# Optimization experiments

Hardware: AMD Instinct MI355X
Metric: run time of the kernel (lower is better)

## Reference

```python
import jax, jax.numpy as jnp
import numpy as np

POOL = 7          # pool_size
RES = 42          # ROIS_resolution
CH = 2048         # backbone output channels (Xception)
GCN_DIM = 256     # gcn_outfeat_dim (== gat_outfeat_dim after head split, heads=1)
HEADS = 1
GAT_CH = 256
ALPHA = 0.1       # APPNP teleport
EPS = 1e-3        # keras BatchNormalization epsilon
CHUNKS = CH // GCN_DIM            # 8 channel chunks per ROI
CNODES = CHUNKS * POOL * POOL     # 392 intra-graph nodes


def _rois():
    # fixed ROI boxes (x, y, w, h) on the 42x42 upsampled map:
    # 3x3 grid of 14x14 cells + two horizontal halves + full image
    c = RES // 3
    r = [(x * c, y * c, c, c) for y in range(3) for x in range(3)]
    r += [(0, 0, RES, RES // 2), (0, RES // 2, RES, RES // 2), (0, 0, RES, RES)]
    return r

ROIS = _rois()
NUM_ROIS = len(ROIS)  # 12


def _gcn_adj(n):
    # spektral GCNConv.preprocess on all-ones adjacency: D^-1/2 (A + I) D^-1/2
    a = np.ones((n, n), np.float32) + np.eye(n, dtype=np.float32)
    d = a.sum(1)
    return jnp.asarray(a / np.sqrt(np.outer(d, d)))

A_INTRA = _gcn_adj(CNODES)        # (392, 392)
A_INTER = _gcn_adj(NUM_ROIS + 1)  # (13, 13)


def _appnp(x, a, w, b):
    # APPNPConv, propagations=1, sigmoid MLP: (1-a)*A@m + a*m
    m = jax.nn.sigmoid(x @ w + b)
    return (1.0 - ALPHA) * jnp.einsum('nm,...mf->...nf', a, m) + ALPHA * m


def _gat(x, a, k, a_self, a_neigh, b):
    # GATConv._call_dense (inference: dropout off); a has add_self_loops folded in
    xp = jnp.einsum('...ni,iho->...nho', x, k)          # (...,N,H,C)
    s = jnp.einsum('...nhi,iho->...nho', xp, a_self)    # (...,N,H,1)
    t = jnp.einsum('...nhi,iho->...nho', xp, a_neigh)   # (...,N,H,1)
    coef = s + jnp.swapaxes(t, -3, -1)                  # (...,N,H,N)
    coef = jax.nn.leaky_relu(coef, 0.2)
    mask = jnp.where(a == 0.0, -1e10, 0.0)              # (N,N) (all-connected here)
    coef = jax.nn.softmax(coef + mask[:, None, :], axis=-1)
    out = jnp.einsum('...nhm,...mhi->...nhi', coef, xp)
    out = out.reshape(out.shape[:-2] + (HEADS * GAT_CH,))  # concat heads
    return jax.nn.elu(out + b)


def _gnn_block(x, a, aw, ab, gk, gs, gn, gb):
    h = _appnp(x, a, aw, ab) + x
    return _gat(h, a, gk, gs, gn, gb) + h


def setup_inputs() -> dict:
    key = jax.random.key(0)
    ks = jax.random.split(key, 8)
    s = 0.05
    return {
        'base_out': jax.random.normal(ks[0], (8, POOL, POOL, CH), jnp.float32),
        'appnp_w': jax.random.normal(ks[1], (GCN_DIM, GCN_DIM), jnp.float32) * s,
        'appnp_b': jnp.zeros((GCN_DIM,), jnp.float32),
        'gat_kernel': jax.random.normal(ks[2], (GCN_DIM, HEADS, GAT_CH), jnp.float32) * s,
        'gat_attn_self': jax.random.normal(ks[3], (GAT_CH, HEADS, 1), jnp.float32) * s,
        'gat_attn_neighs': jax.random.normal(ks[4], (GAT_CH, HEADS, 1), jnp.float32) * s,
        'gat_bias': jnp.zeros((HEADS * GAT_CH,), jnp.float32),
        'pool_feat_w': jax.random.normal(ks[5], (GCN_DIM, 2 * GCN_DIM), jnp.float32) * s,
        'pool_feat_b': jnp.zeros((2 * GCN_DIM,), jnp.float32),
        'pool_attn_w': jax.random.normal(ks[6], (GCN_DIM, 2 * GCN_DIM), jnp.float32) * s,
        'pool_attn_b': jnp.zeros((2 * GCN_DIM,), jnp.float32),
        'bn_gamma': jnp.ones((2 * GCN_DIM,), jnp.float32),
        'bn_beta': jnp.zeros((2 * GCN_DIM,), jnp.float32),
        'bn_mean': jnp.zeros((2 * GCN_DIM,), jnp.float32),
        'bn_var': jnp.ones((2 * GCN_DIM,), jnp.float32),
        'dense_w': jax.random.normal(ks[7], (2 * GCN_DIM, 200), jnp.float32) * s,
        'dense_b': jnp.zeros((200,), jnp.float32),
    }


def reference(base_out, appnp_w, appnp_b, gat_kernel, gat_attn_self, gat_attn_neighs,
              gat_bias, pool_feat_w, pool_feat_b, pool_attn_w, pool_attn_b,
              bn_gamma, bn_beta, bn_mean, bn_var, dense_w, dense_b):
    B = base_out.shape[0]
    # upsample backbone features to ROI resolution
    x0 = jax.image.resize(base_out, (B, RES, RES, CH), 'bilinear')
    # RoiPoolingConv: crop each static ROI and resize to (POOL, POOL)
    pooled = [jax.image.resize(x0[:, y:y + h, x:x + w, :], (B, POOL, POOL, CH), 'bilinear')
              for (x, y, w, h) in ROIS]
    pooled.append(base_out)  # global node (pool_size == base_out spatial dim)
    rois = jnp.stack(pooled, axis=1)  # (B, R+1, 7, 7, CH)
    # _temp_nodes_transform: split channels into CHUNKS, concat along node axis
    nodes = rois.reshape(B, NUM_ROIS + 1, POOL * POOL, CHUNKS, GCN_DIM)
    nodes = nodes.transpose(0, 1, 3, 2, 4).reshape(B, NUM_ROIS + 1, CNODES, GCN_DIM)
    gnn = (appnp_w, appnp_b, gat_kernel, gat_attn_self, gat_attn_neighs, gat_bias)
    # intra-ROI graphs: 13 independent 392-node graphs (batched over (B, R+1))
    x2_intra = _gnn_block(nodes, A_INTRA, *gnn).reshape(B, (NUM_ROIS + 1) * CNODES, GCN_DIM)
    # inter-ROI graphs: 392 independent 13-node graphs
    xt = nodes.transpose(0, 2, 1, 3)  # (B, CNODES, R+1, GCN_DIM)
    x2_inter = _gnn_block(xt, A_INTER, *gnn).reshape(B, CNODES * (NUM_ROIS + 1), GCN_DIM)
    x2 = jnp.concatenate([x2_intra, x2_inter], axis=1)  # (B, 10192, 256)
    # GlobalAttentionPool(512)
    feat = x2 @ pool_feat_w + pool_feat_b
    gate = jax.nn.sigmoid(x2 @ pool_attn_w + pool_attn_b)
    xf = jnp.sum(gate * feat, axis=1)  # (B, 512)
    # BatchNorm (inference) + softmax classifier
    xn = (xf - bn_mean) / jnp.sqrt(bn_var + EPS) * bn_gamma + bn_beta
    return jax.nn.softmax(xn @ dense_w + dense_b, axis=-1)
```

## Files before the change

### kernel.cpp

```cpp
#include <hip/hip_runtime.h>
#include <math.h>


typedef __attribute__((ext_vector_type(8))) short bf16x8;
typedef __attribute__((ext_vector_type(4))) float f32x4;

#define MFMA16x32(a, b, c) __builtin_amdgcn_mfma_f32_16x16x32_bf16((a), (b), (c), 0, 0, 0)

__device__ __forceinline__ float sigmoidf_(float x) { return 1.0f / (1.0f + __expf(-x)); }
__device__ __forceinline__ float leakyf_(float x) { return x >= 0.0f ? x : 0.2f * x; }
__device__ __forceinline__ float eluf_(float x) { return x > 0.0f ? x : __expf(x) - 1.0f; }
__device__ __forceinline__ short f2bf(float f) {
  unsigned u = __builtin_bit_cast(unsigned, f);
  unsigned r = u + 0x7fffu + ((u >> 16) & 1u);
  return (short)(r >> 16);
}
__device__ __forceinline__ float bf2f(short s) {
  unsigned u = ((unsigned)(unsigned short)s) << 16;
  return __builtin_bit_cast(float, u);
}
__device__ __forceinline__ f32x4 fzero4() {
  f32x4 z;
  #pragma unroll
  for (int i = 0; i < 4; ++i) z[i] = 0.0f;
  return z;
}

#define GLDS16(g, l) __builtin_amdgcn_global_load_lds( \
    (const __attribute__((address_space(1))) void*)(g), \
    (__attribute__((address_space(3))) void*)(l), 16, 0, 0)

__global__ __launch_bounds__(256) void prep_k(
    const float* __restrict__ appnp_w, const float* __restrict__ gat_k,
    const float* __restrict__ pf_w, const float* __restrict__ pa_w,
    const float* __restrict__ gat_as, const float* __restrict__ gat_an,
    short* __restrict__ aWhi, short* __restrict__ gkhi,
    short* __restrict__ pwcomb, float* __restrict__ wtab,
    float* __restrict__ was, float* __restrict__ wan) {
  const int bx = blockIdx.x;
  const int tid = threadIdx.x;
  if (bx < 512) {
    const int idx = (bx & 255) * 256 + tid;
    const int k = idx >> 8, n = idx & 255;
    const float* src = (bx < 256) ? appnp_w : gat_k;
    short* dst = (bx < 256) ? aWhi : gkhi;
    dst[(size_t)n * 256 + k] = f2bf(src[(size_t)k * 256 + n]);
  } else if (bx < 1536) {
    const int idx = (bx - 512) * 256 + tid;
    const int n = idx >> 8, k = idx & 255;
    const int p = n >> 4, i = n & 15;
    const int sc = ((p >> 1) << 4) + i;
    const float v = (p & 1) ? pa_w[(size_t)k * 512 + sc] : pf_w[(size_t)k * 512 + sc];
    pwcomb[(size_t)n * 256 + k] = f2bf(v);
  } else if (bx == 1536) {
    const int RX[12] = {0,14,28, 0,14,28, 0,14,28, 0, 0, 0};
    const int RY[12] = {0, 0, 0,14,14,14,28,28,28, 0,21, 0};
    const int RW[12] = {14,14,14,14,14,14,14,14,14,42,42,42};
    const int RH[12] = {14,14,14,14,14,14,14,14,14,21,21,42};
    for (int e = tid; e < 13 * 2 * 49; e += 256) {
      const int roi = e / 98;
      const int rest = e % 98;
      const int axis = rest / 49;
      const int o = (rest % 49) / 7;
      const int ib = rest % 7;
      float wout;
      if (roi == 12) {
        wout = (o == ib) ? 1.0f : 0.0f;
      } else {
        const int start = axis ? RX[roi] : RY[roi];
        const int len = axis ? RW[roi] : RH[roi];
        const float s = (float)len / 7.0f;
        const float oc = (o + 0.5f) * s - 0.5f;
        float wsum = 0.0f, dot = 0.0f;
        for (int j = 0; j < len; ++j) {
          float w = 1.0f - fabsf((float)j - oc) / s;
          if (w <= 0.0f) continue;
          wsum += w;
          const float ic = ((float)(start + j) + 0.5f) / 6.0f - 0.5f;
          const float fl = floorf(ic);
          const int ia = (int)fl;
          const float fr = ic - fl;
          int c0 = ia;     if (c0 < 0) c0 = 0; if (c0 > 6) c0 = 6;
          int c1 = ia + 1; if (c1 < 0) c1 = 0; if (c1 > 6) c1 = 6;
          float u = 0.0f;
          if (c0 == ib) u += 1.0f - fr;
          if (c1 == ib) u += fr;
          dot += w * u;
        }
        wout = dot / wsum;
      }
      wtab[e] = wout;
    }
  } else {
    const int w = tid >> 6, l = tid & 63;
    const int row = (bx - 1537) * 4 + w;
    const float* p = gat_k + (size_t)row * 256;
    float s = 0.0f, t = 0.0f;
    #pragma unroll
    for (int j = 0; j < 4; ++j) {
      const int o = l + j * 64;
      const float v = p[o];
      s = fmaf(v, gat_as[o], s);
      t = fmaf(v, gat_an[o], t);
    }
    #pragma unroll
    for (int off = 32; off; off >>= 1) { s += __shfl_down(s, off); t += __shfl_down(t, off); }
    if (l == 0) { was[row] = s; wan[row] = t; }
  }
}

__global__ __launch_bounds__(256) void nodes_k(const float* __restrict__ base,
                                               const float* __restrict__ wtab,
                                               short* __restrict__ nodes) {
  const int blk = blockIdx.x;
  const int chunk = blk & 7;
  const int br = blk >> 3;
  const int r = br % 13;
  const int b = br / 13;
  const int f = threadIdx.x;
  __shared__ float W49[49][50];
  const float* wv = wtab + (r * 2 + 0) * 49;
  const float* wh = wtab + (r * 2 + 1) * 49;
  for (int e = f; e < 2401; e += 256) {
    const int o = e / 49, in = e % 49;
    W49[o][in] = wv[(o / 7) * 7 + in / 7] * wh[(o % 7) * 7 + in % 7];
  }
  __syncthreads();
  float bv[49];
  const float* bp = base + (size_t)b * 49 * 2048 + chunk * 256 + f;
  #pragma unroll
  for (int in = 0; in < 49; ++in) bv[in] = bp[(size_t)in * 2048];
  const size_t obase = ((size_t)(b * 13 + r) * 392 + chunk * 49) * 256 + f;
  for (int o = 0; o < 49; ++o) {
    float acc = 0.0f;
    #pragma unroll
    for (int in = 0; in < 49; ++in) acc = fmaf(W49[o][in], bv[in], acc);
    nodes[obase + (size_t)o * 256] = f2bf(acc);
  }
}

enum { EP_PLAIN = 0, EP_SIG = 1, EP_POOL = 3 };

template <int EPI>
__global__ __launch_bounds__(256) void gemm_t(
    const short* __restrict__ A, const short* __restrict__ BT,
    const int Kpad, const int nkt, const int Mvalid, const int segRows,
    const float* __restrict__ e0, const float* __restrict__ e1,
    short* __restrict__ Cs, float* __restrict__ xf) {
  const int tid = threadIdx.x;
  const int w = tid >> 6, l = tid & 63;
  const int lr = l & 15, kb = l >> 4;
  const int wr = w >> 1, wc = w & 1;

  int row0, col0, rbase = 0, bseg = 0;
  if constexpr (EPI == EP_POOL) {
    const int bid = blockIdx.x;
    const int eff = (bid & 7) * 640 + (bid >> 3);
    const int mt = eff >> 3, ct = eff & 7;
    row0 = mt * 128; col0 = ct * 128;
    rbase = (mt % 40) * 128;
    bseg = (mt / 40) & 7;
  } else {
    row0 = blockIdx.x * 128; col0 = blockIdx.y * 128;
  }

  __shared__ short As[128][32];
  __shared__ short Bs[128][32];

  const short* ag0 = A + (size_t)(row0 + w * 32 + (l >> 2)) * Kpad + (l & 3) * 8;
  const short* ag1 = ag0 + (size_t)16 * Kpad;
  const short* bg0 = BT + (size_t)(col0 + w * 32 + (l >> 2)) * Kpad + (l & 3) * 8;
  const short* bg1 = bg0 + (size_t)16 * Kpad;
  short* lA0 = &As[w * 32][0];
  short* lA1 = &As[w * 32 + 16][0];
  short* lB0 = &Bs[w * 32][0];
  short* lB1 = &Bs[w * 32 + 16][0];

  f32x4 acc[4][4];
  #pragma unroll
  for (int i = 0; i < 4; ++i)
    #pragma unroll
    for (int j = 0; j < 4; ++j) acc[i][j] = fzero4();

  for (int kt = 0; kt < nkt; ++kt) {
    const int ko = kt * 32;
    __syncthreads();
    GLDS16(ag0 + ko, lA0);
    GLDS16(ag1 + ko, lA1);
    GLDS16(bg0 + ko, lB0);
    GLDS16(bg1 + ko, lB1);
    __syncthreads();
    bf16x8 va[4], vb[4];
    #pragma unroll
    for (int i = 0; i < 4; ++i) va[i] = *(const bf16x8*)&As[wr * 64 + i * 16 + lr][kb * 8];
    #pragma unroll
    for (int j = 0; j < 4; ++j) vb[j] = *(const bf16x8*)&Bs[wc * 64 + j * 16 + lr][kb * 8];
    #pragma unroll
    for (int i = 0; i < 4; ++i)
      #pragma unroll
      for (int j = 0; j < 4; ++j) acc[i][j] = MFMA16x32(va[i], vb[j], acc[i][j]);
  }

  if constexpr (EPI == EP_PLAIN || EPI == EP_SIG) {
    #pragma unroll
    for (int j = 0; j < 4; ++j) {
      const int col = col0 + wc * 64 + j * 16 + lr;
      float bs = 0.0f;
      if constexpr (EPI == EP_SIG) bs = e0[col];
      #pragma unroll
      for (int i = 0; i < 4; ++i) {
        const int row = row0 + wr * 64 + i * 16 + kb * 4;
        #pragma unroll
        for (int r = 0; r < 4; ++r) {
          const int grow = row + r;
          const int lrow = (grow >= segRows) ? grow - segRows : grow;
          if (lrow < Mvalid) {
            float o = acc[i][j][r];
            if constexpr (EPI == EP_SIG) o = sigmoidf_(o + bs);
            Cs[(size_t)grow * 256 + col] = f2bf(o);
          }
        }
      }
    }
  } else {
    #pragma unroll
    for (int jp = 0; jp < 2; ++jp) {
      const int j = jp * 2;
      const int cg = col0 + wc * 64 + j * 16;
      const int realcol = ((cg >> 5) << 4) + lr;
      const float bfv = e0[realcol], bav = e1[realcol];
      float cs = 0.0f;
      #pragma unroll
      for (int i = 0; i < 4; ++i) {
        const int rl = rbase + wr * 64 + i * 16 + kb * 4;
        #pragma unroll
        for (int r = 0; r < 4; ++r) {
          if (rl + r < 5096) {
            const float fv = acc[i][j][r] + bfv;
            const float gv = acc[i][j + 1][r] + bav;
            cs += sigmoidf_(gv) * fv;
          }
        }
      }
      cs += __shfl_xor(cs, 16);
      cs += __shfl_xor(cs, 32);
      if (l < 16) atomicAdd(&xf[(size_t)bseg * 512 + realcol], cs);
    }
  }
}

__global__ __launch_bounds__(256) void attn_setup_k(
    const float* __restrict__ sb, const float* __restrict__ tb,
    unsigned short* __restrict__ ord, float* __restrict__ usr,
    float* __restrict__ vsr, unsigned short* __restrict__ cN,
    float* __restrict__ a1, float* __restrict__ a2) {
  const int g = blockIdx.x;
  const int tid = threadIdx.x;
  __shared__ float t_s[392], s_s[392];
  __shared__ float u_r[392], v_r[392];
  __shared__ float pu_s[393], pv_s[393];
  __shared__ unsigned short cn_s[392];
  __shared__ float red[256];
  const size_t gb = (size_t)g * 392;
  for (int i = tid; i < 392; i += 256) {
    t_s[i] = tb[gb + i];
    s_s[i] = sb[gb + i];
  }
  __syncthreads();
  float lm = -1e30f;
  for (int i = tid; i < 392; i += 256) lm = fmaxf(lm, t_s[i]);
  red[tid] = lm;
  __syncthreads();
  for (int off = 128; off; off >>= 1) {
    if (tid < off) red[tid] = fmaxf(red[tid], red[tid + off]);
    __syncthreads();
  }
  const float tmax = red[0];
  for (int i = tid; i < 392; i += 256) {
    const float ti = t_s[i], si = s_s[i];
    int rt = 0, c = 0;
    for (int j = 0; j < 392; ++j) {
      const float tj = t_s[j];
      rt += (int)((tj < ti) | ((tj == ti) & (j < i)));
      c  += (int)(tj < -si);
    }
    const float u = __expf(ti - tmax);
    const float v = __expf(0.2f * (ti - tmax));
    u_r[rt] = u; v_r[rt] = v;
    ord[gb + rt] = (unsigned short)i;
    usr[gb + rt] = u; vsr[gb + rt] = v;
    cn_s[i] = (unsigned short)c;
    cN[gb + i] = (unsigned short)c;
  }
  __syncthreads();
  if (tid == 0) {
    float r1 = 0.0f, r2 = 0.0f;
    for (int k = 0; k < 392; ++k) {
      pu_s[k] = r1; pv_s[k] = r2;
      r1 += u_r[k]; r2 += v_r[k];
    }
    pu_s[392] = r1; pv_s[392] = r2;
  }
  __syncthreads();
  const float U1 = pu_s[392];
  for (int i = tid; i < 392; i += 256) {
    const float z = s_s[i] + tmax;
    const float c1 = (z < 0.0f) ? __expf(0.8f * z) : 1.0f;
    const float c2 = (z < 0.0f) ? 1.0f : __expf(-0.8f * z);
    const int c = cn_s[i];
    const float den = c1 * (U1 - pu_s[c]) + c2 * pv_s[c];
    a1[gb + i] = c1 / den;
    a2[gb + i] = c2 / den;
  }
}

__global__ __launch_bounds__(256) void attn_seg_k(
    const short* __restrict__ xp, const unsigned short* __restrict__ ord,
    const float* __restrict__ usr, const float* __restrict__ vsr,
    float* __restrict__ SS1, float* __restrict__ SS2) {
  const int g = blockIdx.y, s = blockIdx.x;
  const int f = threadIdx.x;
  const size_t gb = (size_t)g * 392;
  float acc1 = 0.0f, acc2 = 0.0f;
  #pragma unroll
  for (int k = 0; k < 8; ++k) {
    const int r = s * 8 + k;
    const int row = ord[gb + r];
    const float x = bf2f(xp[(gb + row) * 256 + f]);
    acc1 = fmaf(usr[gb + r], x, acc1);
    acc2 = fmaf(vsr[gb + r], x, acc2);
  }
  SS1[((size_t)g * 49 + s) * 256 + f] = acc1;
  SS2[((size_t)g * 49 + s) * 256 + f] = acc2;
}

__global__ __launch_bounds__(256) void attn_scan_k(
    const float* __restrict__ SS1, const float* __restrict__ SS2,
    float* __restrict__ PS1, float* __restrict__ PS2) {
  const int g = blockIdx.x;
  const int f = threadIdx.x;
  float r1 = 0.0f, r2 = 0.0f;
  for (int s = 0; s < 49; ++s) {
    PS1[((size_t)g * 50 + s) * 256 + f] = r1;
    PS2[((size_t)g * 50 + s) * 256 + f] = r2;
    r1 += SS1[((size_t)g * 49 + s) * 256 + f];
    r2 += SS2[((size_t)g * 49 + s) * 256 + f];
  }
  PS1[((size_t)g * 50 + 49) * 256 + f] = r1;
  PS2[((size_t)g * 50 + 49) * 256 + f] = r2;
}

__global__ __launch_bounds__(256) void attn_out_k(
    const short* __restrict__ xp, const unsigned short* __restrict__ ord,
    const float* __restrict__ usr, const float* __restrict__ vsr,
    const unsigned short* __restrict__ cN, const float* __restrict__ a1,
    const float* __restrict__ a2, const float* __restrict__ PS1,
    const float* __restrict__ PS2, const float* __restrict__ bias,
    const short* __restrict__ h, short* __restrict__ x2) {
  const int g = blockIdx.y, bx = blockIdx.x;
  const int f = threadIdx.x;
  const size_t gb = (size_t)g * 392;
  const int bb = g / 13, rr = g % 13;
  const float T1f = PS1[((size_t)g * 50 + 49) * 256 + f];
  const float bf_ = bias[f];
  #pragma unroll
  for (int q = 0; q < 8; ++q) {
    const int n = bx * 8 + q;
    const int c = cN[gb + n];
    const int sN = c >> 3, fine = c & 7;
    float Y1 = PS1[((size_t)g * 50 + sN) * 256 + f];
    float Y2 = PS2[((size_t)g * 50 + sN) * 256 + f];
    for (int k = 0; k < fine; ++k) {
      const int r = sN * 8 + k;
      const int row = ord[gb + r];
      const float x = bf2f(xp[(gb + row) * 256 + f]);
      Y1 = fmaf(usr[gb + r], x, Y1);
      Y2 = fmaf(vsr[gb + r], x, Y2);
    }
    const float num = a1[gb + n] * (T1f - Y1) + a2[gb + n] * Y2;
    const float val = eluf_(num + bf_) + bf2f(h[(gb + n) * 256 + f]);
    x2[((size_t)bb * 5120 + (size_t)rr * 392 + n) * 256 + f] = f2bf(val);
  }
}

__global__ __launch_bounds__(256) void sums_ab_k(const short* __restrict__ m,
    float* __restrict__ Sp, float* __restrict__ Se, int G8) {
  const int f = threadIdx.x;
  if ((int)blockIdx.x < G8) {
    const int g = blockIdx.x >> 3, ch = blockIdx.x & 7;
    const short* p = m + ((size_t)g * 392 + ch * 49) * 256 + f;
    float a0 = 0.0f, a1 = 0.0f, a2 = 0.0f, a3 = 0.0f;
    for (int c = 0; c < 48; c += 4) {
      a0 += bf2f(p[(size_t)(c + 0) * 256]);
      a1 += bf2f(p[(size_t)(c + 1) * 256]);
      a2 += bf2f(p[(size_t)(c + 2) * 256]);
      a3 += bf2f(p[(size_t)(c + 3) * 256]);
    }
    a0 += bf2f(p[(size_t)48 * 256]);
    Sp[((size_t)g * 8 + ch) * 256 + f] = (a0 + a1) + (a2 + a3);
  } else {
    const int g = blockIdx.x - G8;
    const int b = g / 392, c = g % 392;
    const short* p = m + ((size_t)(b * 13) * 392 + c) * 256 + f;
    float acc = 0.0f;
    #pragma unroll
    for (int r = 0; r < 13; ++r) acc += bf2f(p[(size_t)r * 392 * 256]);
    Se[(size_t)g * 256 + f] = acc;
  }
}

__global__ void sums_intra_fin_k(const float* __restrict__ Sp, float* __restrict__ S) {
  const int g = blockIdx.x;
  const int f = threadIdx.x;
  float acc = 0.0f;
  #pragma unroll
  for (int ch = 0; ch < 8; ++ch) acc += Sp[((size_t)g * 8 + ch) * 256 + f];
  S[(size_t)g * 256 + f] = acc;
}

__global__ void h_st_both_k(const short* __restrict__ nodes, const short* __restrict__ m,
    const float* __restrict__ Si, const float* __restrict__ Se,
    const float* __restrict__ was, const float* __restrict__ wan,
    short* __restrict__ h1, short* __restrict__ h2,
    float* __restrict__ sb1, float* __restrict__ tb1,
    float* __restrict__ sb2, float* __restrict__ tb2) {
  const int row = blockIdx.x * 8 + (threadIdx.x >> 5);
  const int f0 = (threadIdx.x & 31) * 8;
  const int g1 = row / 392;
  const int b = row / 5096;
  const int c = row % 392;
  const int g2 = b * 392 + c;
  const size_t e0 = (size_t)row * 256 + f0;
  const bf16x8 mv8 = *(const bf16x8*)(m + e0);
  const bf16x8 nv8 = *(const bf16x8*)(nodes + e0);
  const float* Sp1 = Si + (size_t)g1 * 256 + f0;
  const float* Sp2 = Se + (size_t)g2 * 256 + f0;
  bf16x8 o1, o2;
  float s1 = 0.0f, t1 = 0.0f, s2 = 0.0f, t2 = 0.0f;
  #pragma unroll
  for (int i = 0; i < 8; ++i) {
    const float mv = bf2f(mv8[i]);
    const float base = 0.1f * mv + bf2f(nv8[i]);
    const float hv1 = 0.9f * (Sp1[i] + mv) * (1.0f / 393.0f) + base;
    const float hv2 = 0.9f * (Sp2[i] + mv) * (1.0f / 14.0f) + base;
    o1[i] = f2bf(hv1);
    o2[i] = f2bf(hv2);
    const float wa = was[f0 + i], wn = wan[f0 + i];
    s1 = fmaf(hv1, wa, s1); t1 = fmaf(hv1, wn, t1);
    s2 = fmaf(hv2, wa, s2); t2 = fmaf(hv2, wn, t2);
  }
  *(bf16x8*)(h1 + e0) = o1;
  *(bf16x8*)(h2 + e0) = o2;
  #pragma unroll
  for (int off = 16; off; off >>= 1) {
    s1 += __shfl_xor(s1, off, 32); t1 += __shfl_xor(t1, off, 32);
    s2 += __shfl_xor(s2, off, 32); t2 += __shfl_xor(t2, off, 32);
  }
  if ((threadIdx.x & 31) == 0) {
    sb1[row] = s1; tb1[row] = t1;
    sb2[row] = s2; tb2[row] = t2;
  }
}

__global__ __launch_bounds__(256) void attn_inter_k(const short* __restrict__ xp,
    const float* __restrict__ sb, const float* __restrict__ tb,
    const short* __restrict__ h, const float* __restrict__ bias,
    short* __restrict__ x2, int B) {
  const int g = blockIdx.x;
  const int b = g / 392, c = g % 392;
  const int tid = threadIdx.x;
  __shared__ float xps[13][256];
  __shared__ float e_s[13][14];
  __shared__ float sv[13], tv[13], denom[13];
  __shared__ float tmax_s;
  for (int lin = tid; lin < 13 * 256; lin += 256) {
    const int r = lin >> 8, f = lin & 255;
    xps[r][f] = bf2f(xp[((size_t)(b * 13 + r) * 392 + c) * 256 + f]);
  }
  if (tid < 13) {
    const size_t row = (size_t)(b * 13 + tid) * 392 + c;
    sv[tid] = sb[row];
    tv[tid] = tb[row];
  }
  __syncthreads();
  if (tid == 0) {
    float mx = tv[0];
    for (int r = 1; r < 13; ++r) mx = fmaxf(mx, tv[r]);
    tmax_s = mx;
  }
  __syncthreads();
  if (tid < 169) {
    const int n = tid / 13, mm = tid % 13;
    e_s[n][mm] = __expf(leakyf_(sv[n] + tv[mm]) - leakyf_(sv[n] + tmax_s));
  }
  __syncthreads();
  if (tid < 13) {
    float d = 0.0f;
    for (int mm = 0; mm < 13; ++mm) d += e_s[tid][mm];
    denom[tid] = d;
  }
  __syncthreads();
  const int f = tid;
  for (int n = 0; n < 13; ++n) {
    float acc = 0.0f;
    #pragma unroll
    for (int mm = 0; mm < 13; ++mm) acc = fmaf(e_s[n][mm], xps[mm][f], acc);
    const float o = acc / denom[n];
    const size_t hbase = ((size_t)(b * 13 + n) * 392 + c) * 256 + f;
    x2[(((size_t)(B + b)) * 5120 + (size_t)n * 392 + c) * 256 + f] =
        f2bf(eluf_(o + bias[f]) + bf2f(h[hbase]));
  }
}

__global__ __launch_bounds__(256) void head_k(const float* __restrict__ xf,
    const float* __restrict__ gamma, const float* __restrict__ beta,
    const float* __restrict__ mean, const float* __restrict__ var,
    const float* __restrict__ Wd, const float* __restrict__ bd,
    float* __restrict__ out) {
  const int b = blockIdx.x;
  const int tid = threadIdx.x;
  __shared__ float xn[512];
  __shared__ float red[256];
  for (int i = tid; i < 512; i += 256) {
    const float v = xf[(size_t)b * 512 + i];
    xn[i] = (v - mean[i]) / sqrtf(var[i] + 1e-3f) * gamma[i] + beta[i];
  }
  __syncthreads();
  float logit = -1e30f;
  if (tid < 200) {
    float acc = bd[tid];
    for (int i = 0; i < 512; ++i) acc = fmaf(xn[i], Wd[(size_t)i * 200 + tid], acc);
    logit = acc;
  }
  red[tid] = logit;
  __syncthreads();
  for (int off = 128; off; off >>= 1) {
    if (tid < off) red[tid] = fmaxf(red[tid], red[tid + off]);
    __syncthreads();
  }
  const float mx = red[0];
  __syncthreads();
  const float e = (tid < 200) ? expf(logit - mx) : 0.0f;
  red[tid] = e;
  __syncthreads();
  for (int off = 128; off; off >>= 1) {
    if (tid < off) red[tid] += red[tid + off];
    __syncthreads();
  }
  const float inv = 1.0f / red[0];
  if (tid < 200) out[(size_t)b * 200 + tid] = e * inv;
}

extern "C" void kernel_launch(void* const* d_in, const int* in_sizes, int n_in,
                              void* d_out, int out_size, void* d_ws, size_t ws_size,
                              hipStream_t stream) {
  (void)n_in; (void)out_size; (void)ws_size;
  const float* base    = (const float*)d_in[0];
  const float* appnp_w = (const float*)d_in[1];
  const float* appnp_b = (const float*)d_in[2];
  const float* gat_k   = (const float*)d_in[3];
  const float* gat_as  = (const float*)d_in[4];
  const float* gat_an  = (const float*)d_in[5];
  const float* gat_b   = (const float*)d_in[6];
  const float* pf_w    = (const float*)d_in[7];
  const float* pf_b    = (const float*)d_in[8];
  const float* pa_w    = (const float*)d_in[9];
  const float* pa_b    = (const float*)d_in[10];
  const float* bn_g    = (const float*)d_in[11];
  const float* bn_be   = (const float*)d_in[12];
  const float* bn_mu   = (const float*)d_in[13];
  const float* bn_va   = (const float*)d_in[14];
  const float* dw      = (const float*)d_in[15];
  const float* db      = (const float*)d_in[16];
  float* out = (float*)d_out;

  const int B = in_sizes[0] / (49 * 2048);
  const int G = B * 13;
  const int R = G * 392;
  const int Mt = (R + 127) / 128;
  const int Rpad = Mt * 128;
  const int MP = 2 * B * 5120;

  char* ws = (char*)d_ws;
  size_t off = 0;
  auto alloc = [&](size_t bytes) -> void* {
    void* p = (void*)(ws + off);
    off += (bytes + 255) & ~(size_t)255;
    return p;
  };
  float* wtab   = (float*)alloc((size_t)13 * 2 * 49 * 4);
  short* aWhi   = (short*)alloc((size_t)256 * 256 * 2);
  short* gkhi   = (short*)alloc((size_t)256 * 256 * 2);
  short* pwcomb = (short*)alloc((size_t)1024 * 256 * 2);
  float* was    = (float*)alloc((size_t)256 * 4);
  float* wan    = (float*)alloc((size_t)256 * 4);
  short* nodes  = (short*)alloc((size_t)Rpad * 256 * 2);
  short* mbuf   = (short*)alloc((size_t)R * 256 * 2);
  short* hboth  = (short*)alloc((size_t)2 * Rpad * 256 * 2);
  short* xpboth = (short*)alloc((size_t)2 * Rpad * 256 * 2);
  short* x2buf  = (short*)alloc((size_t)MP * 256 * 2);
  float* Spart  = (float*)alloc((size_t)G * 8 * 256 * 4);
  float* Sintra = (float*)alloc((size_t)G * 256 * 4);
  float* Sinter = (float*)alloc((size_t)B * 392 * 256 * 4);
  float* sbuf   = (float*)alloc((size_t)R * 4);
  float* tbuf   = (float*)alloc((size_t)R * 4);
  float* sbuf2  = (float*)alloc((size_t)R * 4);
  float* tbuf2  = (float*)alloc((size_t)R * 4);
  unsigned short* ordb = (unsigned short*)alloc((size_t)R * 2);
  float* usrb   = (float*)alloc((size_t)R * 4);
  float* vsrb   = (float*)alloc((size_t)R * 4);
  unsigned short* cNb = (unsigned short*)alloc((size_t)R * 2);
  float* a1b    = (float*)alloc((size_t)R * 4);
  float* a2b    = (float*)alloc((size_t)R * 4);
  float* SS1    = (float*)alloc((size_t)G * 49 * 256 * 4);
  float* SS2    = (float*)alloc((size_t)G * 49 * 256 * 4);
  float* PS1    = (float*)alloc((size_t)G * 50 * 256 * 4);
  float* PS2    = (float*)alloc((size_t)G * 50 * 256 * 4);
  float* xf     = (float*)alloc((size_t)B * 512 * 4);

  short* hbuf  = hboth;
  short* hbuf2 = hboth + (size_t)Rpad * 256;
  short* xpbuf  = xpboth;
  short* xpbuf2 = xpboth + (size_t)Rpad * 256;

  hipMemsetAsync(xf, 0, (size_t)B * 512 * 4, stream);
  prep_k<<<1601, 256, 0, stream>>>(appnp_w, gat_k, pf_w, pa_w, gat_as, gat_an,
                                   aWhi, gkhi, pwcomb, wtab, was, wan);
  nodes_k<<<B * 13 * 8, 256, 0, stream>>>(base, wtab, nodes);

  gemm_t<EP_SIG><<<dim3(Mt, 2), 256, 0, stream>>>(nodes, aWhi, 256, 8, R,
      1 << 28, appnp_b, nullptr, mbuf, nullptr);
  sums_ab_k<<<G * 8 + B * 392, 256, 0, stream>>>(mbuf, Spart, Sinter, G * 8);
  sums_intra_fin_k<<<G, 256, 0, stream>>>(Spart, Sintra);

  h_st_both_k<<<R / 8, 256, 0, stream>>>(nodes, mbuf, Sintra, Sinter, was, wan,
                                         hbuf, hbuf2, sbuf, tbuf, sbuf2, tbuf2);

  attn_setup_k<<<G, 256, 0, stream>>>(sbuf, tbuf, ordb, usrb, vsrb, cNb, a1b, a2b);

  gemm_t<EP_PLAIN><<<dim3(2 * Mt, 2), 256, 0, stream>>>(hboth, gkhi, 256, 8, R,
      Rpad, nullptr, nullptr, xpboth, nullptr);

  attn_seg_k<<<dim3(49, G), 256, 0, stream>>>(xpbuf, ordb, usrb, vsrb, SS1, SS2);
  attn_scan_k<<<G, 256, 0, stream>>>(SS1, SS2, PS1, PS2);
  attn_out_k<<<dim3(49, G), 256, 0, stream>>>(xpbuf, ordb, usrb, vsrb, cNb,
      a1b, a2b, PS1, PS2, gat_b, hbuf, x2buf);

  attn_inter_k<<<B * 392, 256, 0, stream>>>(xpbuf2, sbuf2, tbuf2, hbuf2, gat_b, x2buf, B);

  gemm_t<EP_POOL><<<5120, 256, 0, stream>>>(x2buf, pwcomb, 256, 8, 0, 0,
      pf_b, pa_b, nullptr, xf);
  head_k<<<B, 256, 0, stream>>>(xf, bn_g, bn_be, bn_mu, bn_va, dw, db, out);
}
```

Measured before the change: 385.0 us.

## Stage full-K A tile in swizzled LDS and stream B from global with register prefetch

```diff
diff --git a/kernel.cpp b/kernel.cpp
--- a/kernel.cpp
+++ b/kernel.cpp
@@ -25,10 +25,6 @@
   for (int i = 0; i < 4; ++i) z[i] = 0.0f;
   return z;
 }
-
-#define GLDS16(g, l) __builtin_amdgcn_global_load_lds( \
-    (const __attribute__((address_space(1))) void*)(g), \
-    (__attribute__((address_space(3))) void*)(l), 16, 0, 0)
 
 __global__ __launch_bounds__(256) void prep_k(
     const float* __restrict__ appnp_w, const float* __restrict__ gat_k,
@@ -144,7 +140,7 @@
 template <int EPI>
 __global__ __launch_bounds__(256) void gemm_t(
     const short* __restrict__ A, const short* __restrict__ BT,
-    const int Kpad, const int nkt, const int Mvalid, const int segRows,
+    const int Mvalid, const int segRows,
     const float* __restrict__ e0, const float* __restrict__ e1,
     short* __restrict__ Cs, float* __restrict__ xf) {
   const int tid = threadIdx.x;
@@ -164,17 +160,24 @@
     row0 = blockIdx.x * 128; col0 = blockIdx.y * 128;
   }
 
-  __shared__ short As[128][32];
-  __shared__ short Bs[128][32];
-
-  const short* ag0 = A + (size_t)(row0 + w * 32 + (l >> 2)) * Kpad + (l & 3) * 8;
-  const short* ag1 = ag0 + (size_t)16 * Kpad;
-  const short* bg0 = BT + (size_t)(col0 + w * 32 + (l >> 2)) * Kpad + (l & 3) * 8;
-  const short* bg1 = bg0 + (size_t)16 * Kpad;
-  short* lA0 = &As[w * 32][0];
-  short* lA1 = &As[w * 32 + 16][0];
-  short* lB0 = &Bs[w * 32][0];
-  short* lB1 = &Bs[w * 32 + 16][0];
+  __shared__ short As[128][256];
+
+  {
+    const int ar = tid >> 1;
+    const int c0 = (tid & 1) * 128;
+    const short* src = A + (size_t)(row0 + ar) * 256 + c0;
+    const int sw = (ar & 7) << 3;
+    #pragma unroll
+    for (int q = 0; q < 16; ++q) {
+      const bf16x8 v = *(const bf16x8*)(src + q * 8);
+      *(bf16x8*)&As[ar][(c0 + q * 8) ^ sw] = v;
+    }
+  }
+
+  const short* bb0 = BT + (size_t)(col0 + wc * 64 + 0 * 16 + lr) * 256 + kb * 8;
+  const short* bb1 = BT + (size_t)(col0 + wc * 64 + 1 * 16 + lr) * 256 + kb * 8;
+  const short* bb2 = BT + (size_t)(col0 + wc * 64 + 2 * 16 + lr) * 256 + kb * 8;
+  const short* bb3 = BT + (size_t)(col0 + wc * 64 + 3 * 16 + lr) * 256 + kb * 8;
 
   f32x4 acc[4][4];
   #pragma unroll
@@ -182,23 +185,37 @@
     #pragma unroll
     for (int j = 0; j < 4; ++j) acc[i][j] = fzero4();
 
-  for (int kt = 0; kt < nkt; ++kt) {
-    const int ko = kt * 32;
-    __syncthreads();
-    GLDS16(ag0 + ko, lA0);
-    GLDS16(ag1 + ko, lA1);
-    GLDS16(bg0 + ko, lB0);
-    GLDS16(bg1 + ko, lB1);
-    __syncthreads();
-    bf16x8 va[4], vb[4];
-    #pragma unroll
-    for (int i = 0; i < 4; ++i) va[i] = *(const bf16x8*)&As[wr * 64 + i * 16 + lr][kb * 8];
-    #pragma unroll
-    for (int j = 0; j < 4; ++j) vb[j] = *(const bf16x8*)&Bs[wc * 64 + j * 16 + lr][kb * 8];
-    #pragma unroll
-    for (int i = 0; i < 4; ++i)
-      #pragma unroll
-      for (int j = 0; j < 4; ++j) acc[i][j] = MFMA16x32(va[i], vb[j], acc[i][j]);
+  bf16x8 vbA0 = *(const bf16x8*)bb0;
+  bf16x8 vbA1 = *(const bf16x8*)bb1;
+  bf16x8 vbA2 = *(const bf16x8*)bb2;
+  bf16x8 vbA3 = *(const bf16x8*)bb3;
+
+  __syncthreads();
+
+  #pragma unroll
+  for (int kt = 0; kt < 8; ++kt) {
+    bf16x8 vbB0, vbB1, vbB2, vbB3;
+    if (kt + 1 < 8) {
+      const int ko = (kt + 1) * 32;
+      vbB0 = *(const bf16x8*)(bb0 + ko);
+      vbB1 = *(const bf16x8*)(bb1 + ko);
+      vbB2 = *(const bf16x8*)(bb2 + ko);
+      vbB3 = *(const bf16x8*)(bb3 + ko);
+    }
+    bf16x8 va[4];
+    #pragma unroll
+    for (int i = 0; i < 4; ++i) {
+      const int r = wr * 64 + i * 16 + lr;
+      va[i] = *(const bf16x8*)&As[r][(kt * 32 + kb * 8) ^ ((r & 7) << 3)];
+    }
+    #pragma unroll
+    for (int i = 0; i < 4; ++i) {
+      acc[i][0] = MFMA16x32(va[i], vbA0, acc[i][0]);
+      acc[i][1] = MFMA16x32(va[i], vbA1, acc[i][1]);
+      acc[i][2] = MFMA16x32(va[i], vbA2, acc[i][2]);
+      acc[i][3] = MFMA16x32(va[i], vbA3, acc[i][3]);
+    }
+    if (kt + 1 < 8) { vbA0 = vbB0; vbA1 = vbB1; vbA2 = vbB2; vbA3 = vbB3; }
   }
 
   if constexpr (EPI == EP_PLAIN || EPI == EP_SIG) {
@@ -628,8 +645,8 @@
                                    aWhi, gkhi, pwcomb, wtab, was, wan);
   nodes_k<<<B * 13 * 8, 256, 0, stream>>>(base, wtab, nodes);
 
-  gemm_t<EP_SIG><<<dim3(Mt, 2), 256, 0, stream>>>(nodes, aWhi, 256, 8, R,
-      1 << 28, appnp_b, nullptr, mbuf, nullptr);
+  gemm_t<EP_SIG><<<dim3(Mt, 2), 256, 0, stream>>>(nodes, aWhi, R, 1 << 28,
+      appnp_b, nullptr, mbuf, nullptr);
   sums_ab_k<<<G * 8 + B * 392, 256, 0, stream>>>(mbuf, Spart, Sinter, G * 8);
   sums_intra_fin_k<<<G, 256, 0, stream>>>(Spart, Sintra);
 
@@ -638,8 +655,8 @@
 
   attn_setup_k<<<G, 256, 0, stream>>>(sbuf, tbuf, ordb, usrb, vsrb, cNb, a1b, a2b);
 
-  gemm_t<EP_PLAIN><<<dim3(2 * Mt, 2), 256, 0, stream>>>(hboth, gkhi, 256, 8, R,
-      Rpad, nullptr, nullptr, xpboth, nullptr);
+  gemm_t<EP_PLAIN><<<dim3(2 * Mt, 2), 256, 0, stream>>>(hboth, gkhi, R, Rpad,
+      nullptr, nullptr, xpboth, nullptr);
 
   attn_seg_k<<<dim3(49, G), 256, 0, stream>>>(xpbuf, ordb, usrb, vsrb, SS1, SS2);
   attn_scan_k<<<G, 256, 0, stream>>>(SS1, SS2, PS1, PS2);
@@ -648,7 +665,7 @@
 
   attn_inter_k<<<B * 392, 256, 0, stream>>>(xpbuf2, sbuf2, tbuf2, hbuf2, gat_b, x2buf, B);
 
-  gemm_t<EP_POOL><<<5120, 256, 0, stream>>>(x2buf, pwcomb, 256, 8, 0, 0,
+  gemm_t<EP_POOL><<<5120, 256, 0, stream>>>(x2buf, pwcomb, 0, 0,
       pf_b, pa_b, nullptr, xf);
   head_k<<<B, 256, 0, stream>>>(xf, bn_g, bn_be, bn_mu, bn_va, dw, db, out);
 }
```

After: 475.8 us. +23.6%, slower.
